# Optimization experiments

Hardware: AMD Instinct MI355X
Metric: run time of the kernel (lower is better)

The kernel has to match this reference:

```python
import jax, jax.numpy as jnp
import numpy as np

GAMMA = 0.9  # decay (init kwarg)


def setup_inputs() -> dict:
    key = jax.random.key(0)
    k0, k1, k2, k3 = jax.random.split(key, 4)
    B, T, D = 16, 2048, 256
    x = jax.random.normal(k0, (B, T, D), jnp.float32)
    scale = 1.0 / np.sqrt(D)
    Wq = jax.random.normal(k1, (D, D), jnp.float32) * scale
    Wk = jax.random.normal(k2, (D, D), jnp.float32) * scale
    Wv = jax.random.normal(k3, (D, D), jnp.float32) * scale
    return {"x": x, "Wq": Wq, "Wk": Wk, "Wv": Wv}


def reference(x, Wq, Wk, Wv):
    # x: [B, T, D]
    B, T, D = x.shape
    Q = x @ Wq  # [B, T, D]
    K = x @ Wk
    V = x @ Wv

    # Sequential retention recurrence over the [D, D] state:
    #   s[t] = gamma * s[t-1] + K[:, t, :]^T @ V[:, t, :]   (sums over batch, as in source)
    Kt = jnp.swapaxes(K, 0, 1)  # [T, B, D]
    Vt = jnp.swapaxes(V, 0, 1)  # [T, B, D]

    def step(s, kv):
        k_t, v_t = kv  # each [B, D]
        s = GAMMA * s + k_t.T @ v_t  # [D, D]
        return s, s.sum(-1)  # emit row-sum [D]

    # Loop runs t = 1 .. T-1 in the source (s starts at 0); s[0] := s[1].
    init = jnp.zeros((D, D), x.dtype)
    _, rows = jax.lax.scan(step, init, (Kt[1:], Vt[1:]))  # rows: [T-1, D]
    S = jnp.concatenate([rows[:1], rows], axis=0)  # [T, D]

    # Faithful to tf.reshape(S, [-1, seq_len]) then tf.transpose: a reshape-scramble,
    # NOT a plain transpose of S.
    S2 = S.reshape(D, T).T  # [T, D]
    return S2[None, :, :] * Q  # broadcast over batch -> [B, T, D]
```

## Files before the change

### kernel.cpp

```cpp
#include <hip/hip_runtime.h>
#include <hip/hip_bf16.h>
#include <math.h>


#define GAMMA_F 0.9f
#define T_LEN 2048
#define D_DIM 256
#define B_DIM 16
#define NCHUNK 32
#define CHUNK 64

typedef __attribute__((ext_vector_type(8))) short bf16x8;
typedef __attribute__((ext_vector_type(16))) float f32x16;

__device__ inline ushort f2bf(float f) {
    union { float f; unsigned u; } v; v.f = f;
    unsigned r = (v.u + 0x7FFFu + ((v.u >> 16) & 1u)) >> 16;
    return (ushort)r;
}

__global__ __launch_bounds__(256) void k_prep(const float* __restrict__ Wq,
                                              const float* __restrict__ Wk,
                                              const float* __restrict__ Wv,
                                              ushort* __restrict__ WqT,
                                              ushort* __restrict__ WkT,
                                              float* __restrict__ wv_sum) {
    int bid = blockIdx.x;
    int tid = threadIdx.x;
    if (bid < 32) {
        __shared__ float tile[64][68];
        const float* W = (bid < 16) ? Wq : Wk;
        ushort* WT = (bid < 16) ? WqT : WkT;
        int b = bid & 15;
        int k0 = (b & 3) * 64;
        int n0 = (b >> 2) * 64;
        int r = tid >> 4;
        int c4 = (tid & 15) * 4;
#pragma unroll
        for (int i = 0; i < 4; ++i) {
            float4 v = *(const float4*)(W + (size_t)(k0 + r + 16 * i) * D_DIM + n0 + c4);
            *(float4*)&tile[r + 16 * i][c4] = v;
        }
        __syncthreads();
        int n = tid >> 2;
        int j0 = (tid & 3) * 16;
        ushort tmp[16];
#pragma unroll
        for (int i = 0; i < 16; ++i) tmp[i] = f2bf(tile[j0 + i][n]);
        ushort* dst = WT + (size_t)(n0 + n) * D_DIM + k0 + j0;
#pragma unroll
        for (int i = 0; i < 16; ++i) dst[i] = tmp[i];
    } else {
        int j = (bid - 32) * 64 + (tid >> 2);
        int q = tid & 3;
        const float4* row4 = (const float4*)(Wv + (size_t)j * D_DIM + q * 64);
        float s = 0.f;
#pragma unroll
        for (int i = 0; i < 16; ++i) {
            float4 v = row4[i];
            s += v.x + v.y + v.z + v.w;
        }
        s += __shfl_xor(s, 1, 64);
        s += __shfl_xor(s, 2, 64);
        if (q == 0) wv_sum[j] = s;
    }
}

__global__ __launch_bounds__(256) void k_y(const float* __restrict__ x,
                                           const float* __restrict__ wv_sum,
                                           ushort* __restrict__ ybf,
                                           ushort* __restrict__ xbf) {
    int t = blockIdx.x;
    int d = threadIdx.x;
    float wvd = wv_sum[d];
    float xr[B_DIM];
#pragma unroll
    for (int b = 0; b < B_DIM; ++b)
        xr[b] = x[((size_t)b * T_LEN + t) * D_DIM + d];
#pragma unroll
    for (int b = 0; b < B_DIM; ++b)
        xbf[((size_t)b * T_LEN + t) * D_DIM + d] = f2bf(xr[b]);

    __shared__ float red[B_DIM][4];
    int wave = d >> 6, lane = d & 63;
#pragma unroll
    for (int b = 0; b < B_DIM; ++b) {
        float p = xr[b] * wvd;
        for (int o = 32; o > 0; o >>= 1) p += __shfl_down(p, o, 64);
        if (lane == 0) red[b][wave] = p;
    }
    __syncthreads();
    float yv = 0.f;
#pragma unroll
    for (int b = 0; b < B_DIM; ++b) {
        float wb = red[b][0] + red[b][1] + red[b][2] + red[b][3];
        yv += wb * xr[b];
    }
    ybf[(size_t)t * D_DIM + d] = f2bf(yv);
}

__global__ __launch_bounds__(256) void k_gmm(const ushort* __restrict__ ybf,
                                             const ushort* __restrict__ WkT,
                                             float* __restrict__ g) {
    __shared__ ushort As[32 * 64 * 8];
    __shared__ ushort Bs[32 * 64 * 8];
    int mt = blockIdx.x >> 2;
    int nt = blockIdx.x & 3;
    int tid = threadIdx.x, lane = tid & 63, w = tid >> 6;
    int wr = w >> 1, wc = w & 1, l31 = lane & 31, lh = lane >> 5;

#pragma unroll
    for (int i = 0; i < 8; ++i) {
        int slot = tid + 256 * i;
        int r = slot >> 5;
        int s2h = slot & 31;
        int rs = r ^ (s2h & 7);
        *(bf16x8*)&As[(s2h * 64 + rs) * 8] =
            *(const bf16x8*)&ybf[(size_t)(mt * 64 + r) * D_DIM + s2h * 8];
        *(bf16x8*)&Bs[(s2h * 64 + rs) * 8] =
            *(const bf16x8*)&WkT[(size_t)(nt * 64 + r) * D_DIM + s2h * 8];
    }
    __syncthreads();

    f32x16 acc;
#pragma unroll
    for (int e = 0; e < 16; ++e) acc[e] = 0.f;
#pragma unroll
    for (int s = 0; s < 16; ++s) {
        int s2h = s * 2 + lh;
        int ra = (wr * 32 + l31) ^ (s2h & 7);
        int rb = (wc * 32 + l31) ^ (s2h & 7);
        bf16x8 a = *(bf16x8*)&As[(s2h * 64 + ra) * 8];
        bf16x8 b = *(bf16x8*)&Bs[(s2h * 64 + rb) * 8];
        acc = __builtin_amdgcn_mfma_f32_32x32x16_bf16(a, b, acc, 0, 0, 0);
    }
#pragma unroll
    for (int reg = 0; reg < 16; ++reg) {
        int rr = (reg & 3) + 8 * (reg >> 2) + 4 * lh;
        g[(size_t)(mt * 64 + wr * 32 + rr) * D_DIM + nt * 64 + wc * 32 + l31] = acc[reg];
    }
}

__global__ void k_scanA(const float* __restrict__ g, float* __restrict__ loc,
                        float* __restrict__ carry) {
    int c = blockIdx.x;
    int d = threadIdx.x;
    float acc = 0.f;
    int base = c * CHUNK;
#pragma unroll
    for (int o8 = 0; o8 < 8; ++o8) {
        float v[8];
#pragma unroll
        for (int j = 0; j < 8; ++j) {
            int t = base + o8 * 8 + j;
            v[j] = (t == 0) ? 0.f : g[(size_t)t * D_DIM + d];
        }
#pragma unroll
        for (int j = 0; j < 8; ++j) {
            acc = GAMMA_F * acc + v[j];
            loc[(size_t)(base + o8 * 8 + j) * D_DIM + d] = acc;
        }
    }
    carry[(size_t)c * D_DIM + d] = acc;
}

__global__ __launch_bounds__(256) void k_S2P(const float* __restrict__ loc,
                                             const float* __restrict__ carry,
                                             float* __restrict__ S2) {
    int tp = blockIdx.x;
    int r = threadIdx.x;
    int src = (tp == 0) ? 1 : tp;
    int c = src >> 6, o = src & 63;
    const float g64 = 1.1790184577738601e-03f;
    float p = 0.f;
    for (int j = 0; j < c; ++j)
        p = p * g64 + carry[(size_t)j * D_DIM + r];
    const float log2g = -0.15200309344504995f;
    float gp = exp2f((float)(o + 1) * log2g);
    float Aval = loc[(size_t)src * D_DIM + r] + gp * p;
    int trow = ((tp & 7) << 8) + r;
    int dcol = tp >> 3;
    S2[(size_t)trow * D_DIM + dcol] = Aval;
}

__global__ __launch_bounds__(256) void k_qgemm(const ushort* __restrict__ xbf,
                                               const ushort* __restrict__ WqT,
                                               const float* __restrict__ S2,
                                               float* __restrict__ out) {
    __shared__ ushort As[8 * 128 * 8];
    __shared__ ushort Bs[8 * 128 * 8];
    int bid = blockIdx.x;
    int mb = bid >> 1;
    int nb = bid & 1;
    int tid = threadIdx.x;
    int lane = tid & 63, w = tid >> 6;
    int wr = w >> 1, wc = w & 1;
    int l31 = lane & 31, lh = lane >> 5;

    f32x16 acc[2][2];
#pragma unroll
    for (int i = 0; i < 2; ++i)
#pragma unroll
        for (int j = 0; j < 2; ++j)
#pragma unroll
            for (int e = 0; e < 16; ++e) acc[i][j][e] = 0.f;

    int r = tid >> 1;
    int h0 = tid & 1;
    const ushort* ag = xbf + (size_t)(mb * 128 + r) * D_DIM + h0 * 32;
    const ushort* bg = WqT + (size_t)(nb * 128 + r) * D_DIM + h0 * 32;

    for (int kb = 0; kb < 4; ++kb) {
#pragma unroll
        for (int j = 0; j < 4; ++j) {
            bf16x8 av = *(const bf16x8*)(ag + kb * 64 + j * 8);
            *(bf16x8*)&As[((h0 * 4 + j) * 128 + r) * 8] = av;
            bf16x8 bv = *(const bf16x8*)(bg + kb * 64 + j * 8);
            *(bf16x8*)&Bs[((h0 * 4 + j) * 128 + r) * 8] = bv;
        }
        __syncthreads();
#pragma unroll
        for (int s = 0; s < 4; ++s) {
            int c0 = (s * 2 + lh) * 128;
            bf16x8 a0 = *(bf16x8*)&As[(c0 + wr * 64 + l31) * 8];
            bf16x8 a1 = *(bf16x8*)&As[(c0 + wr * 64 + 32 + l31) * 8];
            bf16x8 b0 = *(bf16x8*)&Bs[(c0 + wc * 64 + l31) * 8];
            bf16x8 b1 = *(bf16x8*)&Bs[(c0 + wc * 64 + 32 + l31) * 8];
            acc[0][0] = __builtin_amdgcn_mfma_f32_32x32x16_bf16(a0, b0, acc[0][0], 0, 0, 0);
            acc[0][1] = __builtin_amdgcn_mfma_f32_32x32x16_bf16(a0, b1, acc[0][1], 0, 0, 0);
            acc[1][0] = __builtin_amdgcn_mfma_f32_32x32x16_bf16(a1, b0, acc[1][0], 0, 0, 0);
            acc[1][1] = __builtin_amdgcn_mfma_f32_32x32x16_bf16(a1, b1, acc[1][1], 0, 0, 0);
        }
        __syncthreads();
    }

    int t_base = (mb & 15) * 128;
    size_t row_base = (size_t)mb * 128;
#pragma unroll
    for (int mi = 0; mi < 2; ++mi) {
#pragma unroll
        for (int ni = 0; ni < 2; ++ni) {
            int gn = nb * 128 + wc * 64 + ni * 32 + l31;
#pragma unroll
            for (int reg = 0; reg < 16; ++reg) {
                int rr = (reg & 3) + 8 * (reg >> 2) + 4 * lh;
                int m = wr * 64 + mi * 32 + rr;
                float s2v = S2[(size_t)(t_base + m) * D_DIM + gn];
                out[(row_base + m) * D_DIM + gn] = acc[mi][ni][reg] * s2v;
            }
        }
    }
}

extern "C" void kernel_launch(void* const* d_in, const int* in_sizes, int n_in,
                              void* d_out, int out_size, void* d_ws, size_t ws_size,
                              hipStream_t stream) {
    const float* x  = (const float*)d_in[0];
    const float* Wq = (const float*)d_in[1];
    const float* Wk = (const float*)d_in[2];
    const float* Wv = (const float*)d_in[3];
    float* out = (float*)d_out;

    float* ws = (float*)d_ws;
    float* g      = ws;
    float* loc    = g + 524288;
    float* S2     = loc + 524288;
    float* wv_sum = S2 + 524288;
    float* carry  = wv_sum + 256;
    ushort* WqT   = (ushort*)(carry + 8192);
    ushort* WkT   = WqT + 65536;
    ushort* ybf   = WkT + 65536;
    ushort* xbf   = ybf + 524288;

    k_prep<<<36, 256, 0, stream>>>(Wq, Wk, Wv, WqT, WkT, wv_sum);
    k_y<<<T_LEN, 256, 0, stream>>>(x, wv_sum, ybf, xbf);
    k_gmm<<<128, 256, 0, stream>>>(ybf, WkT, g);
    k_scanA<<<NCHUNK, 256, 0, stream>>>(g, loc, carry);
    k_S2P<<<T_LEN, 256, 0, stream>>>(loc, carry, S2);
    k_qgemm<<<(B_DIM * T_LEN / 128) * 2, 256, 0, stream>>>(xbf, WqT, S2, out);
}
```

Before: 128.9 us.

## Fuse x bf16 conversion into Q GEMM and shorten scan chunks

Removes the intermediate bf16 copy of x, converting fp32 x to bf16 while staging tiles in the Q GEMM, which avoids a full write and re-read of the activations. The chunked decay scan is split into many more short chunks so more blocks run in parallel, and the carry combine is truncated to the last 32 chunks since older contributions decay to negligible values. The GEMM now reads wider fp32 data and does the conversion inline, and the truncation introduces a tiny approximation error.

```diff
diff --git a/kernel.cpp b/kernel.cpp
--- a/kernel.cpp
+++ b/kernel.cpp
@@ -7,8 +7,6 @@
 #define T_LEN 2048
 #define D_DIM 256
 #define B_DIM 16
-#define NCHUNK 32
-#define CHUNK 64
 
 typedef __attribute__((ext_vector_type(8))) short bf16x8;
 typedef __attribute__((ext_vector_type(16))) float f32x16;
@@ -68,8 +66,7 @@
 
 __global__ __launch_bounds__(256) void k_y(const float* __restrict__ x,
                                            const float* __restrict__ wv_sum,
-                                           ushort* __restrict__ ybf,
-                                           ushort* __restrict__ xbf) {
+                                           ushort* __restrict__ ybf) {
     int t = blockIdx.x;
     int d = threadIdx.x;
     float wvd = wv_sum[d];
@@ -77,9 +74,6 @@
 #pragma unroll
     for (int b = 0; b < B_DIM; ++b)
         xr[b] = x[((size_t)b * T_LEN + t) * D_DIM + d];
-#pragma unroll
-    for (int b = 0; b < B_DIM; ++b)
-        xbf[((size_t)b * T_LEN + t) * D_DIM + d] = f2bf(xr[b]);
 
     __shared__ float red[B_DIM][4];
     int wave = d >> 6, lane = d & 63;
@@ -145,21 +139,17 @@
                         float* __restrict__ carry) {
     int c = blockIdx.x;
     int d = threadIdx.x;
+    float v[8];
+#pragma unroll
+    for (int j = 0; j < 8; ++j) {
+        int t = c * 8 + j;
+        v[j] = (t == 0) ? 0.f : g[(size_t)t * D_DIM + d];
+    }
     float acc = 0.f;
-    int base = c * CHUNK;
-#pragma unroll
-    for (int o8 = 0; o8 < 8; ++o8) {
-        float v[8];
-#pragma unroll
-        for (int j = 0; j < 8; ++j) {
-            int t = base + o8 * 8 + j;
-            v[j] = (t == 0) ? 0.f : g[(size_t)t * D_DIM + d];
-        }
-#pragma unroll
-        for (int j = 0; j < 8; ++j) {
-            acc = GAMMA_F * acc + v[j];
-            loc[(size_t)(base + o8 * 8 + j) * D_DIM + d] = acc;
-        }
+#pragma unroll
+    for (int j = 0; j < 8; ++j) {
+        acc = GAMMA_F * acc + v[j];
+        loc[(size_t)(c * 8 + j) * D_DIM + d] = acc;
     }
     carry[(size_t)c * D_DIM + d] = acc;
 }
@@ -170,11 +160,12 @@
     int tp = blockIdx.x;
     int r = threadIdx.x;
     int src = (tp == 0) ? 1 : tp;
-    int c = src >> 6, o = src & 63;
-    const float g64 = 1.1790184577738601e-03f;
+    int c = src >> 3, o = src & 7;
+    const float g8 = 0.43046721f;
+    int j0 = c - 32; if (j0 < 0) j0 = 0;
     float p = 0.f;
-    for (int j = 0; j < c; ++j)
-        p = p * g64 + carry[(size_t)j * D_DIM + r];
+    for (int j = j0; j < c; ++j)
+        p = p * g8 + carry[(size_t)j * D_DIM + r];
     const float log2g = -0.15200309344504995f;
     float gp = exp2f((float)(o + 1) * log2g);
     float Aval = loc[(size_t)src * D_DIM + r] + gp * p;
@@ -183,7 +174,7 @@
     S2[(size_t)trow * D_DIM + dcol] = Aval;
 }
 
-__global__ __launch_bounds__(256) void k_qgemm(const ushort* __restrict__ xbf,
+__global__ __launch_bounds__(256) void k_qgemm(const float* __restrict__ x,
                                                const ushort* __restrict__ WqT,
                                                const float* __restrict__ S2,
                                                float* __restrict__ out) {
@@ -207,14 +198,19 @@
 
     int r = tid >> 1;
     int h0 = tid & 1;
-    const ushort* ag = xbf + (size_t)(mb * 128 + r) * D_DIM + h0 * 32;
+    const float* ag = x + (size_t)(mb * 128 + r) * D_DIM + h0 * 32;
     const ushort* bg = WqT + (size_t)(nb * 128 + r) * D_DIM + h0 * 32;
 
     for (int kb = 0; kb < 4; ++kb) {
 #pragma unroll
         for (int j = 0; j < 4; ++j) {
-            bf16x8 av = *(const bf16x8*)(ag + kb * 64 + j * 8);
-            *(bf16x8*)&As[((h0 * 4 + j) * 128 + r) * 8] = av;
+            float4 v0 = *(const float4*)(ag + kb * 64 + j * 8);
+            float4 v1 = *(const float4*)(ag + kb * 64 + j * 8 + 4);
+            ushort4 p0, p1;
+            p0.x = f2bf(v0.x); p0.y = f2bf(v0.y); p0.z = f2bf(v0.z); p0.w = f2bf(v0.w);
+            p1.x = f2bf(v1.x); p1.y = f2bf(v1.y); p1.z = f2bf(v1.z); p1.w = f2bf(v1.w);
+            *(ushort4*)&As[((h0 * 4 + j) * 128 + r) * 8] = p0;
+            *(ushort4*)&As[((h0 * 4 + j) * 128 + r) * 8 + 4] = p1;
             bf16x8 bv = *(const bf16x8*)(bg + kb * 64 + j * 8);
             *(bf16x8*)&Bs[((h0 * 4 + j) * 128 + r) * 8] = bv;
         }
@@ -267,15 +263,14 @@
     float* S2     = loc + 524288;
     float* wv_sum = S2 + 524288;
     float* carry  = wv_sum + 256;
-    ushort* WqT   = (ushort*)(carry + 8192);
+    ushort* WqT   = (ushort*)(carry + 65536);
     ushort* WkT   = WqT + 65536;
     ushort* ybf   = WkT + 65536;
-    ushort* xbf   = ybf + 524288;
 
     k_prep<<<36, 256, 0, stream>>>(Wq, Wk, Wv, WqT, WkT, wv_sum);
-    k_y<<<T_LEN, 256, 0, stream>>>(x, wv_sum, ybf, xbf);
+    k_y<<<T_LEN, 256, 0, stream>>>(x, wv_sum, ybf);
     k_gmm<<<128, 256, 0, stream>>>(ybf, WkT, g);
-    k_scanA<<<NCHUNK, 256, 0, stream>>>(g, loc, carry);
+    k_scanA<<<256, 256, 0, stream>>>(g, loc, carry);
     k_S2P<<<T_LEN, 256, 0, stream>>>(loc, carry, S2);
-    k_qgemm<<<(B_DIM * T_LEN / 128) * 2, 256, 0, stream>>>(xbf, WqT, S2, out);
-}
+    k_qgemm<<<(B_DIM * T_LEN / 128) * 2, 256, 0, stream>>>(x, WqT, S2, out);
+}
```

Result: no change. 130.7 us (+1.4%).
